# Kernel tuning notes

Hardware: AMD Instinct MI355X
Metric: run time of the kernel (lower is better)

The kernel has to match this reference:

```python
import jax, jax.numpy as jnp
import numpy as np

B, H, V, L = 1024, 2048, 8192, 8


def setup_inputs() -> dict:
    key = jax.random.key(0)
    k1, k2, k3, k4 = jax.random.split(key, 4)
    state = jax.random.normal(k1, (B, H), dtype=jnp.float32)
    token = jax.random.randint(k2, (B,), 0, V, dtype=jnp.int64)
    ih = jax.random.normal(k3, (L, V, H), dtype=jnp.float32) * 0.02
    hh = jax.random.normal(k4, (L, H, H), dtype=jnp.float32) * 0.02
    return {"state": state, "token": token, "ih": ih, "hh": hh}


def reference(state, token, ih, hh):
    # Per layer: state = tanh(state + (state @ hh[i]) * ih[i][token])
    # ih[i][token]: gather -> [B, H]; state @ hh[i]: [B,H]@[H,H] -> [B,H]
    def step(s, layer_params):
        hh_i, ih_i = layer_params
        gate = ih_i[token]                      # [B, H] embedding gather
        s = jnp.tanh(s + (s @ hh_i) * gate)     # fused mul-add-tanh
        return s, None

    state, _ = jax.lax.scan(step, state, (hh, ih))
    return state
```

## Files before the change

### kernel.cpp

```cpp
#include <hip/hip_runtime.h>
#include <hip/hip_bf16.h>

#define B_DIM 1024
#define H_DIM 2048
#define V_DIM 8192
#define L_DIM 8

typedef __attribute__((ext_vector_type(8))) __bf16 bf16x8;
typedef __attribute__((ext_vector_type(4))) __bf16 bf16x4;
typedef __attribute__((ext_vector_type(4))) float f32x4;
typedef unsigned short u16;

#define ASM_BARRIER() asm volatile("s_barrier" ::: "memory")
#define WAIT_VM12() asm volatile("s_waitcnt vmcnt(12)" ::: "memory")
#define WAIT_VM8() asm volatile("s_waitcnt vmcnt(8)" ::: "memory")
#define WAIT_VM4() asm volatile("s_waitcnt vmcnt(4)" ::: "memory")
#define WAIT_VM0() asm volatile("s_waitcnt vmcnt(0)" ::: "memory")

__device__ __forceinline__ void async_copy16(const void* g, void* l) {
  __builtin_amdgcn_global_load_lds(
      (const unsigned int __attribute__((address_space(1)))*)g,
      (unsigned int __attribute__((address_space(3)))*)l,
      16, 0, 0);
}

__global__ __launch_bounds__(256) void rnn_conv_state(
    const float4* __restrict__ in, bf16x4* __restrict__ out) {
  int i = blockIdx.x * 256 + threadIdx.x;
  float4 v = in[i];
  bf16x4 o;
  o.x = (__bf16)v.x; o.y = (__bf16)v.y; o.z = (__bf16)v.z; o.w = (__bf16)v.w;
  out[i] = o;
}

__global__ __launch_bounds__(256) void rnn_hh_transpose_all(
    const float* __restrict__ hh, __bf16* __restrict__ hhT) {
  int bid = blockIdx.x;
  int l = bid >> 10;
  int t = bid & 1023;
  int k0 = (t >> 5) << 6;
  int n0 = (t & 31) << 6;
  __shared__ __bf16 tile[64][67];
  int tid = threadIdx.x;
  const float* hh_l = hh + ((size_t)l << 22);
  __bf16* hhT_l = hhT + ((size_t)l << 22);
  {
    int r = tid >> 2;
    int c = (tid & 3) << 4;
    const float4* src = (const float4*)(hh_l + (size_t)(k0 + r) * H_DIM + n0 + c);
#pragma unroll
    for (int q = 0; q < 4; q++) {
      float4 v = src[q];
      tile[r][c + q * 4 + 0] = (__bf16)v.x;
      tile[r][c + q * 4 + 1] = (__bf16)v.y;
      tile[r][c + q * 4 + 2] = (__bf16)v.z;
      tile[r][c + q * 4 + 3] = (__bf16)v.w;
    }
  }
  __syncthreads();
  {
    int n = tid >> 2;
    int kq = (tid & 3) << 4;
    alignas(16) u16 tmp[16];
#pragma unroll
    for (int j = 0; j < 16; j++) {
      __bf16 b = tile[kq + j][n];
      tmp[j] = *(const u16*)&b;
    }
    uint4* dst = (uint4*)(hhT_l + (size_t)(n0 + n) * H_DIM + k0 + kq);
    dst[0] = *(uint4*)(tmp);
    dst[1] = *(uint4*)(tmp + 8);
  }
}

__global__ __launch_bounds__(256) void rnn_layer_pipe(
    const __bf16* __restrict__ A, const __bf16* __restrict__ Bt,
    const float* __restrict__ S, const float* __restrict__ ih_l,
    const int* __restrict__ token,
    float* __restrict__ OutF, __bf16* __restrict__ OutB) {
  constexpr int K = H_DIM;
  constexpr int NT = K / 64;
  __shared__ __align__(16) __bf16 As[4][64 * 64];
  __shared__ __align__(16) __bf16 Bs[4][64 * 64];

  int bid = blockIdx.x;
  int x = bid & 7;
  int rest = bid >> 3;
  int mi = (x & 1) * 8 + (rest & 7);
  int ni = (x >> 1) * 8 + (rest >> 3);
  int bm0 = mi * 64;
  int bn0 = ni * 64;

  int tid = threadIdx.x;
  int w = tid >> 6;
  int lane = tid & 63;
  int rsub = lane >> 3;
  int csw = (lane & 7) ^ rsub;

  const __bf16* pA0 = A + (size_t)(bm0 + (w * 2 + 0) * 8 + rsub) * K + csw * 8;
  const __bf16* pA1 = A + (size_t)(bm0 + (w * 2 + 1) * 8 + rsub) * K + csw * 8;
  const __bf16* pB0 = Bt + (size_t)(bn0 + (w * 2 + 0) * 8 + rsub) * K + csw * 8;
  const __bf16* pB1 = Bt + (size_t)(bn0 + (w * 2 + 1) * 8 + rsub) * K + csw * 8;
  int slot0 = (w * 2 + 0) * 512;
  int slot1 = (w * 2 + 1) * 512;

  int wm = (w >> 1) * 32;
  int wn = (w & 1) * 32;
  int col = lane & 15;
  int quad = lane >> 4;
  int c7 = lane & 7;

  f32x4 acc[2][2] = {};

  auto issue = [&](int buf, int kt) {
    int ko = kt * 64;
    async_copy16(pA0 + ko, &As[buf][slot0]);
    async_copy16(pA1 + ko, &As[buf][slot1]);
    async_copy16(pB0 + ko, &Bs[buf][slot0]);
    async_copy16(pB1 + ko, &Bs[buf][slot1]);
  };
  auto compute = [&](int buf) {
#pragma unroll
    for (int ks = 0; ks < 2; ks++) {
      int cc = ks * 4 + quad;
      bf16x8 a0 = *(const bf16x8*)(&As[buf][(wm + 0 + col) * 64 + ((cc ^ c7) * 8)]);
      bf16x8 a1 = *(const bf16x8*)(&As[buf][(wm + 16 + col) * 64 + ((cc ^ c7) * 8)]);
      bf16x8 b0 = *(const bf16x8*)(&Bs[buf][(wn + 0 + col) * 64 + ((cc ^ c7) * 8)]);
      bf16x8 b1 = *(const bf16x8*)(&Bs[buf][(wn + 16 + col) * 64 + ((cc ^ c7) * 8)]);
      acc[0][0] = __builtin_amdgcn_mfma_f32_16x16x32_bf16(a0, b0, acc[0][0], 0, 0, 0);
      acc[0][1] = __builtin_amdgcn_mfma_f32_16x16x32_bf16(a0, b1, acc[0][1], 0, 0, 0);
      acc[1][0] = __builtin_amdgcn_mfma_f32_16x16x32_bf16(a1, b0, acc[1][0], 0, 0, 0);
      acc[1][1] = __builtin_amdgcn_mfma_f32_16x16x32_bf16(a1, b1, acc[1][1], 0, 0, 0);
    }
  };

  issue(0, 0);
  issue(1, 1);
  issue(2, 2);
  for (int t = 0; t < NT - 3; ++t) {
    issue((t + 3) & 3, t + 3);
    WAIT_VM12();
    ASM_BARRIER();
    compute(t & 3);
    ASM_BARRIER();
  }
  WAIT_VM8();
  ASM_BARRIER();
  compute((NT - 3) & 3);
  ASM_BARRIER();
  WAIT_VM4();
  ASM_BARRIER();
  compute((NT - 2) & 3);
  ASM_BARRIER();
  WAIT_VM0();
  ASM_BARRIER();
  compute((NT - 1) & 3);

#pragma unroll
  for (int mt = 0; mt < 2; mt++) {
#pragma unroll
    for (int reg = 0; reg < 4; reg++) {
      int b = bm0 + wm + mt * 16 + quad * 4 + reg;
      int tok = token[b];
      const float* ihrow = ih_l + (size_t)tok * H_DIM;
      size_t rowoff = (size_t)b * H_DIM;
#pragma unroll
      for (int nt = 0; nt < 2; nt++) {
        int h = bn0 + wn + nt * 16 + col;
        float g = ihrow[h];
        float sv = S[rowoff + h];
        float v = tanhf(fmaf(acc[mt][nt][reg], g, sv));
        OutF[rowoff + h] = v;
        OutB[rowoff + h] = (__bf16)v;
      }
    }
  }
}

extern "C" void kernel_launch(void* const* d_in, const int* in_sizes, int n_in,
                              void* d_out, int out_size, void* d_ws, size_t ws_size,
                              hipStream_t stream) {
  const float* state = (const float*)d_in[0];
  const int* token = (const int*)d_in[1];
  const float* ih = (const float*)d_in[2];
  const float* hh = (const float*)d_in[3];

  char* ws = (char*)d_ws;
  __bf16* hhT = (__bf16*)ws;
  float* F0 = (float*)(ws + 67108864);
  float* F1 = (float*)(ws + 75497472);
  __bf16* Sb0 = (__bf16*)(ws + 83886080);
  __bf16* Sb1 = (__bf16*)(ws + 88080384);

  rnn_hh_transpose_all<<<8192, 256, 0, stream>>>(hh, hhT);
  rnn_conv_state<<<2048, 256, 0, stream>>>((const float4*)state, (bf16x4*)Sb0);

  const float* Sprev = state;
  for (int l = 0; l < L_DIM; l++) {
    const __bf16* hhT_l = hhT + ((size_t)l << 22);
    const float* ih_l = ih + ((size_t)l << 24);
    const __bf16* Acur = (l & 1) ? Sb1 : Sb0;
    __bf16* outB = (l & 1) ? Sb0 : Sb1;
    float* outF = (l == L_DIM - 1) ? (float*)d_out : ((l & 1) ? F1 : F0);
    rnn_layer_pipe<<<512, 256, 0, stream>>>(Acur, hhT_l, Sprev, ih_l, token, outF, outB);
    Sprev = outF;
  }
}
```

Measured before the change: 923.4 us.

## Fuse transpose, state conversion and all layers into one cooperative persistent kernel

Replaces the ten separate launches (weight transpose, state conversion, eight layer GEMMs) with a single cooperative kernel of 512 blocks. Grid-wide syncs separate the preprocessing from the layers and each layer from the next. This removes per-launch overhead and gaps between kernels. In exchange, the 8192-block transpose becomes a 16-iteration loop inside each of the 512 blocks, which may lower parallelism for that phase. Grid sync cost and the occupancy limits of a cooperative launch also apply, and the old multi-launch path remains as a fallback if the cooperative launch fails.

After: 2.127 ms. 2.3x slower.

```diff
diff --git a/kernel.cpp b/kernel.cpp
--- a/kernel.cpp
+++ b/kernel.cpp
@@ -1,5 +1,8 @@
 #include <hip/hip_runtime.h>
 #include <hip/hip_bf16.h>
+#include <hip/hip_cooperative_groups.h>
+
+namespace cg = cooperative_groups;
 
 #define B_DIM 1024
 #define H_DIM 2048
@@ -22,6 +25,190 @@
       (const unsigned int __attribute__((address_space(1)))*)g,
       (unsigned int __attribute__((address_space(3)))*)l,
       16, 0, 0);
+}
+
+__global__ __launch_bounds__(256, 2) void rnn_fused(
+    const float* __restrict__ state, const int* __restrict__ token,
+    const float* __restrict__ ih, const float* __restrict__ hh,
+    __bf16* __restrict__ hhT, float* __restrict__ F0, float* __restrict__ F1,
+    __bf16* __restrict__ Sb0, __bf16* __restrict__ Sb1,
+    float* __restrict__ dout) {
+  __shared__ __align__(16) __bf16 As[4][4096];
+  __shared__ __align__(16) __bf16 Bs[4][4096];
+  cg::grid_group grid = cg::this_grid();
+  int bid = blockIdx.x;
+  int tid = threadIdx.x;
+
+  {
+    __bf16(*tile)[67] = (__bf16(*)[67])(&As[0][0]);
+    for (int i = 0; i < 16; ++i) {
+      int g = bid * 16 + i;
+      int l = g >> 10;
+      int t = g & 1023;
+      int k0 = (t >> 5) << 6;
+      int n0 = (t & 31) << 6;
+      const float* hh_l = hh + ((size_t)l << 22);
+      __bf16* hhT_l = hhT + ((size_t)l << 22);
+      if (i) __syncthreads();
+      {
+        int r = tid >> 2;
+        int c = (tid & 3) << 4;
+        const float4* src =
+            (const float4*)(hh_l + (size_t)(k0 + r) * H_DIM + n0 + c);
+#pragma unroll
+        for (int q = 0; q < 4; q++) {
+          float4 v = src[q];
+          tile[r][c + q * 4 + 0] = (__bf16)v.x;
+          tile[r][c + q * 4 + 1] = (__bf16)v.y;
+          tile[r][c + q * 4 + 2] = (__bf16)v.z;
+          tile[r][c + q * 4 + 3] = (__bf16)v.w;
+        }
+      }
+      __syncthreads();
+      {
+        int n = tid >> 2;
+        int kq = (tid & 3) << 4;
+        alignas(16) u16 tmp[16];
+#pragma unroll
+        for (int j = 0; j < 16; j++) {
+          __bf16 b = tile[kq + j][n];
+          tmp[j] = *(const u16*)&b;
+        }
+        uint4* dst = (uint4*)(hhT_l + (size_t)(n0 + n) * H_DIM + k0 + kq);
+        dst[0] = *(uint4*)(tmp);
+        dst[1] = *(uint4*)(tmp + 8);
+      }
+    }
+  }
+  {
+    const float4* in = (const float4*)state;
+    bf16x4* out = (bf16x4*)Sb0;
+    int base = bid * 256 + tid;
+#pragma unroll
+    for (int it = 0; it < 4; ++it) {
+      int i = base + it * 131072;
+      float4 v = in[i];
+      bf16x4 o;
+      o.x = (__bf16)v.x; o.y = (__bf16)v.y; o.z = (__bf16)v.z; o.w = (__bf16)v.w;
+      out[i] = o;
+    }
+  }
+  __threadfence();
+  grid.sync();
+  __threadfence();
+
+  int x = bid & 7;
+  int rest = bid >> 3;
+  int mi = (x & 1) * 8 + (rest & 7);
+  int ni = (x >> 1) * 8 + (rest >> 3);
+  int bm0 = mi * 64;
+  int bn0 = ni * 64;
+
+  int w = tid >> 6;
+  int lane = tid & 63;
+  int rsub = lane >> 3;
+  int csw = (lane & 7) ^ rsub;
+  int slot0 = (w * 2 + 0) * 512;
+  int slot1 = (w * 2 + 1) * 512;
+  int wm = (w >> 1) * 32;
+  int wn = (w & 1) * 32;
+  int col = lane & 15;
+  int quad = lane >> 4;
+  int c7 = lane & 7;
+
+  size_t offA0 = (size_t)(bm0 + (w * 2 + 0) * 8 + rsub) * H_DIM + csw * 8;
+  size_t offA1 = (size_t)(bm0 + (w * 2 + 1) * 8 + rsub) * H_DIM + csw * 8;
+  size_t offB0 = (size_t)(bn0 + (w * 2 + 0) * 8 + rsub) * H_DIM + csw * 8;
+  size_t offB1 = (size_t)(bn0 + (w * 2 + 1) * 8 + rsub) * H_DIM + csw * 8;
+
+#pragma unroll 1
+  for (int l = 0; l < L_DIM; ++l) {
+    const __bf16* Acur = (l & 1) ? Sb1 : Sb0;
+    const __bf16* Bt = hhT + ((size_t)l << 22);
+    const float* S = (l == 0) ? state : ((l & 1) ? F0 : F1);
+    const float* ih_l = ih + ((size_t)l << 24);
+    float* OutF = (l == L_DIM - 1) ? dout : ((l & 1) ? F1 : F0);
+    __bf16* OutB = (l & 1) ? Sb0 : Sb1;
+    const bool lastL = (l == L_DIM - 1);
+
+    const __bf16* pA0 = Acur + offA0;
+    const __bf16* pA1 = Acur + offA1;
+    const __bf16* pB0 = Bt + offB0;
+    const __bf16* pB1 = Bt + offB1;
+
+    constexpr int NT = H_DIM / 64;
+    f32x4 acc[2][2] = {};
+
+    auto issue = [&](int buf, int kt) {
+      int ko = kt * 64;
+      async_copy16(pA0 + ko, &As[buf][slot0]);
+      async_copy16(pA1 + ko, &As[buf][slot1]);
+      async_copy16(pB0 + ko, &Bs[buf][slot0]);
+      async_copy16(pB1 + ko, &Bs[buf][slot1]);
+    };
+    auto compute = [&](int buf) {
+#pragma unroll
+      for (int ks = 0; ks < 2; ks++) {
+        int cc = ks * 4 + quad;
+        bf16x8 a0 = *(const bf16x8*)(&As[buf][(wm + 0 + col) * 64 + ((cc ^ c7) * 8)]);
+        bf16x8 a1 = *(const bf16x8*)(&As[buf][(wm + 16 + col) * 64 + ((cc ^ c7) * 8)]);
+        bf16x8 b0 = *(const bf16x8*)(&Bs[buf][(wn + 0 + col) * 64 + ((cc ^ c7) * 8)]);
+        bf16x8 b1 = *(const bf16x8*)(&Bs[buf][(wn + 16 + col) * 64 + ((cc ^ c7) * 8)]);
+        acc[0][0] = __builtin_amdgcn_mfma_f32_16x16x32_bf16(a0, b0, acc[0][0], 0, 0, 0);
+        acc[0][1] = __builtin_amdgcn_mfma_f32_16x16x32_bf16(a0, b1, acc[0][1], 0, 0, 0);
+        acc[1][0] = __builtin_amdgcn_mfma_f32_16x16x32_bf16(a1, b0, acc[1][0], 0, 0, 0);
+        acc[1][1] = __builtin_amdgcn_mfma_f32_16x16x32_bf16(a1, b1, acc[1][1], 0, 0, 0);
+      }
+    };
+
+    issue(0, 0);
+    issue(1, 1);
+    issue(2, 2);
+    for (int t = 0; t < NT - 3; ++t) {
+      issue((t + 3) & 3, t + 3);
+      WAIT_VM12();
+      ASM_BARRIER();
+      compute(t & 3);
+      ASM_BARRIER();
+    }
+    WAIT_VM8();
+    ASM_BARRIER();
+    compute((NT - 3) & 3);
+    ASM_BARRIER();
+    WAIT_VM4();
+    ASM_BARRIER();
+    compute((NT - 2) & 3);
+    ASM_BARRIER();
+    WAIT_VM0();
+    ASM_BARRIER();
+    compute((NT - 1) & 3);
+
+#pragma unroll
+    for (int mt = 0; mt < 2; mt++) {
+#pragma unroll
+      for (int reg = 0; reg < 4; reg++) {
+        int b = bm0 + wm + mt * 16 + quad * 4 + reg;
+        int tok = token[b];
+        const float* ihrow = ih_l + (size_t)tok * H_DIM;
+        size_t rowoff = (size_t)b * H_DIM;
+#pragma unroll
+        for (int nt = 0; nt < 2; nt++) {
+          int h = bn0 + wn + nt * 16 + col;
+          float g = ihrow[h];
+          float sv = S[rowoff + h];
+          float v = tanhf(fmaf(acc[mt][nt][reg], g, sv));
+          OutF[rowoff + h] = v;
+          if (!lastL) OutB[rowoff + h] = (__bf16)v;
+        }
+      }
+    }
+
+    if (!lastL) {
+      __threadfence();
+      grid.sync();
+      __threadfence();
+    }
+  }
 }
 
 __global__ __launch_bounds__(256) void rnn_conv_state(
@@ -191,18 +378,27 @@
   float* F1 = (float*)(ws + 75497472);
   __bf16* Sb0 = (__bf16*)(ws + 83886080);
   __bf16* Sb1 = (__bf16*)(ws + 88080384);
-
-  rnn_hh_transpose_all<<<8192, 256, 0, stream>>>(hh, hhT);
-  rnn_conv_state<<<2048, 256, 0, stream>>>((const float4*)state, (bf16x4*)Sb0);
-
-  const float* Sprev = state;
-  for (int l = 0; l < L_DIM; l++) {
-    const __bf16* hhT_l = hhT + ((size_t)l << 22);
-    const float* ih_l = ih + ((size_t)l << 24);
-    const __bf16* Acur = (l & 1) ? Sb1 : Sb0;
-    __bf16* outB = (l & 1) ? Sb0 : Sb1;
-    float* outF = (l == L_DIM - 1) ? (float*)d_out : ((l & 1) ? F1 : F0);
-    rnn_layer_pipe<<<512, 256, 0, stream>>>(Acur, hhT_l, Sprev, ih_l, token, outF, outB);
-    Sprev = outF;
-  }
-}
+  float* dout = (float*)d_out;
+
+  void* args[] = {(void*)&state, (void*)&token, (void*)&ih, (void*)&hh,
+                  (void*)&hhT,   (void*)&F0,    (void*)&F1, (void*)&Sb0,
+                  (void*)&Sb1,   (void*)&dout};
+  hipError_t err = hipLaunchCooperativeKernel(
+      (const void*)rnn_fused, dim3(512), dim3(256), args, 0, stream);
+
+  if (err != hipSuccess) {
+    rnn_hh_transpose_all<<<8192, 256, 0, stream>>>(hh, hhT);
+    rnn_conv_state<<<2048, 256, 0, stream>>>((const float4*)state, (bf16x4*)Sb0);
+    const float* Sprev = state;
+    for (int l = 0; l < L_DIM; l++) {
+      const __bf16* hhT_l = hhT + ((size_t)l << 22);
+      const float* ih_l = ih + ((size_t)l << 24);
+      const __bf16* Acur = (l & 1) ? Sb1 : Sb0;
+      __bf16* outB = (l & 1) ? Sb0 : Sb1;
+      float* outF = (l == L_DIM - 1) ? (float*)d_out : ((l & 1) ? F1 : F0);
+      rnn_layer_pipe<<<512, 256, 0, stream>>>(Acur, hhT_l, Sprev, ih_l, token,
+                                              outF, (__bf16*)outB);
+      Sprev = outF;
+    }
+  }
+}
```
